# Optimization experiments

Measured on AMD Instinct MI355X. Metric: run time of the kernel, lower is better.

Reference implementation:

```python
import jax, jax.numpy as jnp
import numpy as np

K = 3  # kernel_size / number of adjacency partitions


def setup_inputs() -> dict:
    key = jax.random.key(0)
    k1, k2, k3 = jax.random.split(key, 3)
    N, C_in, T, V = 64, 64, 300, 25
    C_out = 64
    x = jax.random.normal(k1, (N, C_in, T, V), dtype=jnp.float32)
    A = jax.random.uniform(k2, (K, V, V), dtype=jnp.float32)
    W = jax.random.normal(k3, (C_in, K * C_out), dtype=jnp.float32) * 0.05
    b = jnp.zeros((K * C_out,), dtype=jnp.float32)
    return {"x": x, "A": A, "W": W, "b": b}


def reference(x, A, W, b):
    # 1x1 conv (channels_first) == per-position channel projection
    # x: [N, C_in, T, V], W: [C_in, K*C_out] -> y: [N, K*C_out, T, V]
    y = jnp.einsum('nitv,io->notv', x, W) + b[None, :, None, None]
    N, KC, T, V = y.shape
    C = KC // K
    y = y.reshape(N, K, C, T, V)
    # graph adjacency aggregation: [N,K,C,T,V] x [K,V,W] -> [N,C,T,W]
    out = jnp.einsum('nkctv,kvw->nctw', y, A)
    return (out, A)
```

## Files before the change

### kernel.cpp

```cpp
#include <hip/hip_runtime.h>
#include <hip/hip_bf16.h>


#define TT 3
#define TCHUNKS 100
#define NB 64
#define CI 64
#define TDIM 300
#define VDIM 25
#define CO 64
#define KK 3

#define XROWS (TT*32)
#define SMEM_BYTES (XROWS*128)

#define WBUF_BYTES (KK*4*2*64*16)
#define ABUF_BYTES (KK*2*64*16)

typedef __attribute__((ext_vector_type(8))) short bf16x8;
typedef __attribute__((ext_vector_type(4))) float f32x4;
typedef __attribute__((ext_vector_type(4))) int i32x4;
typedef __attribute__((ext_vector_type(4), aligned(4))) float f32x4u;

__device__ __forceinline__ unsigned int pack2(float lo, float hi) {
    __hip_bfloat162 h = __float22bfloat162_rn(make_float2(lo, hi));
    unsigned int u;
    __builtin_memcpy(&u, &h, 4);
    return u;
}
__device__ __forceinline__ unsigned short f2bf(float f) {
    __hip_bfloat16 h = __float2bfloat16(f);
    unsigned short u;
    __builtin_memcpy(&u, &h, 2);
    return u;
}

__global__ void sgcn_prep(const float* __restrict__ A, const float* __restrict__ W,
                          unsigned int* __restrict__ wbuf, unsigned int* __restrict__ abuf,
                          float* __restrict__ outA) {
    int id = blockIdx.x * 256 + threadIdx.x;
    if (id < KK * 4 * 2 * 64) {
        int l  = id & 63;
        int h  = (id >> 6) & 1;
        int wq = (id >> 7) & 3;
        int k  = id >> 9;
        int c  = wq * 16 + (l & 15);
        int ib = (l >> 4) * 8 + h * 32;
        unsigned int pk[4];
        #pragma unroll
        for (int j = 0; j < 4; ++j)
            pk[j] = pack2(W[(size_t)(ib + 2*j)     * (KK*CO) + k*CO + c],
                          W[(size_t)(ib + 2*j + 1) * (KK*CO) + k*CO + c]);
        *(uint4*)(wbuf + id * 4) = make_uint4(pk[0], pk[1], pk[2], pk[3]);
    }
    if (id < KK * 2 * 64) {
        int l  = id & 63;
        int nt = (id >> 6) & 1;
        int k  = id >> 7;
        int w  = nt * 16 + (l & 15);
        int vb = (l >> 4) * 8;
        unsigned int pk[4];
        #pragma unroll
        for (int j = 0; j < 4; ++j) {
            int v0 = vb + 2*j, v1 = v0 + 1;
            unsigned short u0 = (v0 < VDIM && w < VDIM) ? f2bf(A[k*VDIM*VDIM + v0*VDIM + w]) : (unsigned short)0;
            unsigned short u1 = (v1 < VDIM && w < VDIM) ? f2bf(A[k*VDIM*VDIM + v1*VDIM + w]) : (unsigned short)0;
            pk[j] = (unsigned int)u0 | ((unsigned int)u1 << 16);
        }
        *(uint4*)(abuf + id * 4) = make_uint4(pk[0], pk[1], pk[2], pk[3]);
    }
    if (id < KK * VDIM * VDIM) outA[id] = A[id];
}

__global__ __launch_bounds__(256, 4) void sgcn_fused(
    const float* __restrict__ x, const float* __restrict__ b,
    const unsigned int* __restrict__ wbuf, const unsigned int* __restrict__ abuf,
    float* __restrict__ out)
{
    __shared__ __align__(16) char smem[SMEM_BYTES];
    const int tid  = threadIdx.x;
    const int lane = tid & 63;
    const int wid  = tid >> 6;
    const int n    = blockIdx.y;
    const int t0   = blockIdx.x * TT;
    const int l15  = lane & 15;
    const int g    = lane >> 4;
    const int i0   = g * 8;
    const int c    = wid * 16 + l15;

    f32x4 q0[3], q1[3];
    #pragma unroll
    for (int j = 0; j < 3; ++j) {
        int id  = tid + j * 256;
        int i2  = id / 24;
        int rem = id - i2 * 24;
        int t   = rem >> 3;
        int grp = rem & 7;
        const float* pc0 = x + (((size_t)n * CI + 2*i2) * TDIM + (t0 + t)) * VDIM + 4*grp;
        const float* pc1 = pc0 + TDIM * VDIM;
        q0[j] = (f32x4){0.f, 0.f, 0.f, 0.f};
        q1[j] = (f32x4){0.f, 0.f, 0.f, 0.f};
        if (grp < 6) {
            q0[j] = *(const f32x4u*)pc0;
            q1[j] = *(const f32x4u*)pc1;
        } else if (grp == 6) {
            q0[j].x = pc0[0];
            q1[j].x = pc1[0];
        }
    }

    bf16x8 WB[KK][2], AB[KK][2];
    float bv[KK];
    #pragma unroll
    for (int k = 0; k < KK; ++k) {
        WB[k][0] = *(const bf16x8*)(wbuf + (((k*4 + wid)*2 + 0)*64 + lane)*4);
        WB[k][1] = *(const bf16x8*)(wbuf + (((k*4 + wid)*2 + 1)*64 + lane)*4);
        AB[k][0] = *(const bf16x8*)(abuf + ((k*2 + 0)*64 + lane)*4);
        AB[k][1] = *(const bf16x8*)(abuf + ((k*2 + 1)*64 + lane)*4);
        bv[k]    = b[k*CO + c];
    }

    #pragma unroll
    for (int j = 0; j < 3; ++j) {
        int id  = tid + j * 256;
        int i2  = id / 24;
        int rem = id - i2 * 24;
        int t   = rem >> 3;
        int grp = rem & 7;
        int rr0 = ((grp & 1) << 4) + ((grp >> 1) << 2);
        int rbase = t * 32 + rr0;
        int m   = rr0 & 7;
        #pragma unroll
        for (int p = 0; p < 4; ++p) {
            int fx = ((m + p) & 7) ^ t;
            int addr = (rbase + p) * 128 + ((4*i2) ^ (fx << 4));
            *(unsigned int*)(smem + addr) = pack2(q0[j][p], q1[j][p]);
        }
    }
    __syncthreads();

    const size_t cs = (size_t)TDIM * VDIM;
    #pragma unroll
    for (int t = 0; t < TT; ++t) {
        int j0 = t*32 + l15;
        int j1 = j0 + 16;
        const char* p0 = smem + j0*128;
        const char* p1 = smem + j1*128;
        int fx = ((l15 & 7) ^ t) << 4;
        bf16x8 A00 = *(const bf16x8*)(p0 + ((2*i0)      ^ fx));
        bf16x8 A01 = *(const bf16x8*)(p0 + ((2*i0 + 64) ^ fx));
        bf16x8 A10 = *(const bf16x8*)(p1 + ((2*i0)      ^ fx));
        bf16x8 A11 = *(const bf16x8*)(p1 + ((2*i0 + 64) ^ fx));

        f32x4 accA = {0.f, 0.f, 0.f, 0.f};
        f32x4 accB = {0.f, 0.f, 0.f, 0.f};
        #pragma unroll
        for (int k = 0; k < KK; ++k) {
            f32x4 D0 = {bv[k], bv[k], bv[k], bv[k]};
            f32x4 D1 = D0;
            D0 = __builtin_amdgcn_mfma_f32_16x16x32_bf16(A00, WB[k][0], D0, 0, 0, 0);
            D0 = __builtin_amdgcn_mfma_f32_16x16x32_bf16(A01, WB[k][1], D0, 0, 0, 0);
            D1 = __builtin_amdgcn_mfma_f32_16x16x32_bf16(A10, WB[k][0], D1, 0, 0, 0);
            D1 = __builtin_amdgcn_mfma_f32_16x16x32_bf16(A11, WB[k][1], D1, 0, 0, 0);
            i32x4 pav = {(int)pack2(D0.x, D0.y), (int)pack2(D0.z, D0.w),
                         (int)pack2(D1.x, D1.y), (int)pack2(D1.z, D1.w)};
            bf16x8 PA = __builtin_bit_cast(bf16x8, pav);
            accA = __builtin_amdgcn_mfma_f32_16x16x32_bf16(PA, AB[k][0], accA, 0, 0, 0);
            accB = __builtin_amdgcn_mfma_f32_16x16x32_bf16(PA, AB[k][1], accB, 0, 0, 0);
        }
        size_t base = (((size_t)n * CO + (wid*16 + 4*g)) * TDIM + (t0 + t)) * VDIM + l15;
        out[base]        = accA.x;
        out[base + cs]   = accA.y;
        out[base + 2*cs] = accA.z;
        out[base + 3*cs] = accA.w;
        if (l15 < VDIM - 16) {
            size_t base2 = base + 16;
            out[base2]        = accB.x;
            out[base2 + cs]   = accB.y;
            out[base2 + 2*cs] = accB.z;
            out[base2 + 3*cs] = accB.w;
        }
    }
}

extern "C" void kernel_launch(void* const* d_in, const int* in_sizes, int n_in,
                              void* d_out, int out_size, void* d_ws, size_t ws_size,
                              hipStream_t stream) {
    const float* x = (const float*)d_in[0];
    const float* A = (const float*)d_in[1];
    const float* W = (const float*)d_in[2];
    const float* b = (const float*)d_in[3];
    float* out = (float*)d_out;

    unsigned int* wbuf = (unsigned int*)d_ws;
    unsigned int* abuf = (unsigned int*)((char*)d_ws + WBUF_BYTES);

    const size_t out_elems = (size_t)NB * CO * TDIM * VDIM;
    sgcn_prep<<<8, 256, 0, stream>>>(A, W, wbuf, abuf, out + out_elems);

    dim3 grid(TCHUNKS, NB);
    sgcn_fused<<<grid, 256, 0, stream>>>(x, b, wbuf, abuf, out);
}
```

Baseline: 64.85 us.

## Double-buffer x tiles in shared memory to overlap next-chunk loads with compute

Each block now covers two chunks of six timesteps and uses two shared-memory buffers. Global loads for the second chunk are issued before the first chunk's MFMA work, then written to the second buffer afterwards. The aim is to hide global load latency behind compute and to cut the number of blocks. In exchange it needs more registers, 48KB of LDS per block and a lower launch-bounds occupancy of 2 blocks, with only 1600 blocks in the grid.

```diff
diff --git a/kernel.cpp b/kernel.cpp
--- a/kernel.cpp
+++ b/kernel.cpp
@@ -2,8 +2,9 @@
 #include <hip/hip_bf16.h>
 
 
-#define TT 3
-#define TCHUNKS 100
+#define TT 6
+#define NCHUNK 2
+#define GRIDX 25
 #define NB 64
 #define CI 64
 #define TDIM 300
@@ -72,42 +73,62 @@
     if (id < KK * VDIM * VDIM) outA[id] = A[id];
 }
 
-__global__ __launch_bounds__(256, 4) void sgcn_fused(
+__global__ __launch_bounds__(256, 2) void sgcn_fused(
     const float* __restrict__ x, const float* __restrict__ b,
     const unsigned int* __restrict__ wbuf, const unsigned int* __restrict__ abuf,
     float* __restrict__ out)
 {
-    __shared__ __align__(16) char smem[SMEM_BYTES];
+    __shared__ __align__(16) char smem[2][SMEM_BYTES];
     const int tid  = threadIdx.x;
     const int lane = tid & 63;
     const int wid  = tid >> 6;
     const int n    = blockIdx.y;
-    const int t0   = blockIdx.x * TT;
+    const int t0   = blockIdx.x * (TT * NCHUNK);
     const int l15  = lane & 15;
     const int g    = lane >> 4;
     const int i0   = g * 8;
     const int c    = wid * 16 + l15;
 
-    f32x4 q0[3], q1[3];
-    #pragma unroll
-    for (int j = 0; j < 3; ++j) {
-        int id  = tid + j * 256;
-        int i2  = id / 24;
-        int rem = id - i2 * 24;
-        int t   = rem >> 3;
-        int grp = rem & 7;
-        const float* pc0 = x + (((size_t)n * CI + 2*i2) * TDIM + (t0 + t)) * VDIM + 4*grp;
-        const float* pc1 = pc0 + TDIM * VDIM;
-        q0[j] = (f32x4){0.f, 0.f, 0.f, 0.f};
-        q1[j] = (f32x4){0.f, 0.f, 0.f, 0.f};
-        if (grp < 6) {
-            q0[j] = *(const f32x4u*)pc0;
-            q1[j] = *(const f32x4u*)pc1;
-        } else if (grp == 6) {
-            q0[j].x = pc0[0];
-            q1[j].x = pc1[0];
-        }
-    }
+    float q0[6][4], q1[6][4];
+
+    #define STAGE_LOAD(TBASE)                                                        \
+        _Pragma("unroll")                                                            \
+        for (int j = 0; j < 6; ++j) {                                                \
+            int id  = tid + j * 256;                                                 \
+            int i2  = id / 48;                                                       \
+            int rem = id - i2 * 48;                                                  \
+            int t   = rem >> 3;                                                      \
+            int grp = rem & 7;                                                       \
+            const float* pc0 = x + (((size_t)n * CI + 2*i2) * TDIM + ((TBASE) + t)) * VDIM + 4*grp; \
+            const float* pc1 = pc0 + TDIM * VDIM;                                    \
+            f32x4 a0 = {0.f, 0.f, 0.f, 0.f};                                         \
+            f32x4 a1 = {0.f, 0.f, 0.f, 0.f};                                         \
+            if (grp < 6)      { a0 = *(const f32x4u*)pc0; a1 = *(const f32x4u*)pc1; }\
+            else if (grp == 6){ a0.x = pc0[0];            a1.x = pc1[0]; }           \
+            q0[j][0]=a0.x; q0[j][1]=a0.y; q0[j][2]=a0.z; q0[j][3]=a0.w;              \
+            q1[j][0]=a1.x; q1[j][1]=a1.y; q1[j][2]=a1.z; q1[j][3]=a1.w;              \
+        }
+
+    #define STAGE_WRITE(BUF)                                                         \
+        _Pragma("unroll")                                                            \
+        for (int j = 0; j < 6; ++j) {                                                \
+            int id  = tid + j * 256;                                                 \
+            int i2  = id / 48;                                                       \
+            int rem = id - i2 * 48;                                                  \
+            int t   = rem >> 3;                                                      \
+            int grp = rem & 7;                                                       \
+            int rr0 = ((grp & 1) << 4) + ((grp >> 1) << 2);                          \
+            int rbase = t * 32 + rr0;                                                \
+            int m   = rr0 & 7;                                                       \
+            _Pragma("unroll")                                                        \
+            for (int p = 0; p < 4; ++p) {                                            \
+                int fx = ((m + p) & 7) ^ t;                                          \
+                int addr = (rbase + p) * 128 + ((4*i2) ^ (fx << 4));                 \
+                *(unsigned int*)((BUF) + addr) = pack2(q0[j][p], q1[j][p]);          \
+            }                                                                        \
+        }
+
+    STAGE_LOAD(t0);
 
     bf16x8 WB[KK][2], AB[KK][2];
     float bv[KK];
@@ -120,67 +141,67 @@
         bv[k]    = b[k*CO + c];
     }
 
+    STAGE_WRITE(&smem[0][0]);
+    __syncthreads();
+
+    const size_t cs = (size_t)TDIM * VDIM;
+
     #pragma unroll
-    for (int j = 0; j < 3; ++j) {
-        int id  = tid + j * 256;
-        int i2  = id / 24;
-        int rem = id - i2 * 24;
-        int t   = rem >> 3;
-        int grp = rem & 7;
-        int rr0 = ((grp & 1) << 4) + ((grp >> 1) << 2);
-        int rbase = t * 32 + rr0;
-        int m   = rr0 & 7;
+    for (int ch = 0; ch < NCHUNK; ++ch) {
+        const char* rbuf = &smem[ch][0];
+        const int   tg0  = t0 + ch * TT;
+
+        if (ch == 0) STAGE_LOAD(t0 + TT);
+
         #pragma unroll
-        for (int p = 0; p < 4; ++p) {
-            int fx = ((m + p) & 7) ^ t;
-            int addr = (rbase + p) * 128 + ((4*i2) ^ (fx << 4));
-            *(unsigned int*)(smem + addr) = pack2(q0[j][p], q1[j][p]);
-        }
-    }
-    __syncthreads();
-
-    const size_t cs = (size_t)TDIM * VDIM;
-    #pragma unroll
-    for (int t = 0; t < TT; ++t) {
-        int j0 = t*32 + l15;
-        int j1 = j0 + 16;
-        const char* p0 = smem + j0*128;
-        const char* p1 = smem + j1*128;
-        int fx = ((l15 & 7) ^ t) << 4;
-        bf16x8 A00 = *(const bf16x8*)(p0 + ((2*i0)      ^ fx));
-        bf16x8 A01 = *(const bf16x8*)(p0 + ((2*i0 + 64) ^ fx));
-        bf16x8 A10 = *(const bf16x8*)(p1 + ((2*i0)      ^ fx));
-        bf16x8 A11 = *(const bf16x8*)(p1 + ((2*i0 + 64) ^ fx));
-
-        f32x4 accA = {0.f, 0.f, 0.f, 0.f};
-        f32x4 accB = {0.f, 0.f, 0.f, 0.f};
-        #pragma unroll
-        for (int k = 0; k < KK; ++k) {
-            f32x4 D0 = {bv[k], bv[k], bv[k], bv[k]};
-            f32x4 D1 = D0;
-            D0 = __builtin_amdgcn_mfma_f32_16x16x32_bf16(A00, WB[k][0], D0, 0, 0, 0);
-            D0 = __builtin_amdgcn_mfma_f32_16x16x32_bf16(A01, WB[k][1], D0, 0, 0, 0);
-            D1 = __builtin_amdgcn_mfma_f32_16x16x32_bf16(A10, WB[k][0], D1, 0, 0, 0);
-            D1 = __builtin_amdgcn_mfma_f32_16x16x32_bf16(A11, WB[k][1], D1, 0, 0, 0);
-            i32x4 pav = {(int)pack2(D0.x, D0.y), (int)pack2(D0.z, D0.w),
-                         (int)pack2(D1.x, D1.y), (int)pack2(D1.z, D1.w)};
-            bf16x8 PA = __builtin_bit_cast(bf16x8, pav);
-            accA = __builtin_amdgcn_mfma_f32_16x16x32_bf16(PA, AB[k][0], accA, 0, 0, 0);
-            accB = __builtin_amdgcn_mfma_f32_16x16x32_bf16(PA, AB[k][1], accB, 0, 0, 0);
-        }
-        size_t base = (((size_t)n * CO + (wid*16 + 4*g)) * TDIM + (t0 + t)) * VDIM + l15;
-        out[base]        = accA.x;
-        out[base + cs]   = accA.y;
-        out[base + 2*cs] = accA.z;
-        out[base + 3*cs] = accA.w;
-        if (l15 < VDIM - 16) {
-            size_t base2 = base + 16;
-            out[base2]        = accB.x;
-            out[base2 + cs]   = accB.y;
-            out[base2 + 2*cs] = accB.z;
-            out[base2 + 3*cs] = accB.w;
-        }
-    }
+        for (int t = 0; t < TT; ++t) {
+            int j0 = t*32 + l15;
+            int j1 = j0 + 16;
+            const char* p0 = rbuf + j0*128;
+            const char* p1 = rbuf + j1*128;
+            int fx = ((l15 & 7) ^ t) << 4;
+            bf16x8 A00 = *(const bf16x8*)(p0 + ((2*i0)      ^ fx));
+            bf16x8 A01 = *(const bf16x8*)(p0 + ((2*i0 + 64) ^ fx));
+            bf16x8 A10 = *(const bf16x8*)(p1 + ((2*i0)      ^ fx));
+            bf16x8 A11 = *(const bf16x8*)(p1 + ((2*i0 + 64) ^ fx));
+
+            f32x4 accA = {0.f, 0.f, 0.f, 0.f};
+            f32x4 accB = {0.f, 0.f, 0.f, 0.f};
+            #pragma unroll
+            for (int k = 0; k < KK; ++k) {
+                f32x4 D0 = {bv[k], bv[k], bv[k], bv[k]};
+                f32x4 D1 = D0;
+                D0 = __builtin_amdgcn_mfma_f32_16x16x32_bf16(A00, WB[k][0], D0, 0, 0, 0);
+                D0 = __builtin_amdgcn_mfma_f32_16x16x32_bf16(A01, WB[k][1], D0, 0, 0, 0);
+                D1 = __builtin_amdgcn_mfma_f32_16x16x32_bf16(A10, WB[k][0], D1, 0, 0, 0);
+                D1 = __builtin_amdgcn_mfma_f32_16x16x32_bf16(A11, WB[k][1], D1, 0, 0, 0);
+                i32x4 pav = {(int)pack2(D0.x, D0.y), (int)pack2(D0.z, D0.w),
+                             (int)pack2(D1.x, D1.y), (int)pack2(D1.z, D1.w)};
+                bf16x8 PA = __builtin_bit_cast(bf16x8, pav);
+                accA = __builtin_amdgcn_mfma_f32_16x16x32_bf16(PA, AB[k][0], accA, 0, 0, 0);
+                accB = __builtin_amdgcn_mfma_f32_16x16x32_bf16(PA, AB[k][1], accB, 0, 0, 0);
+            }
+            size_t base = (((size_t)n * CO + (wid*16 + 4*g)) * TDIM + (tg0 + t)) * VDIM + l15;
+            out[base]        = accA.x;
+            out[base + cs]   = accA.y;
+            out[base + 2*cs] = accA.z;
+            out[base + 3*cs] = accA.w;
+            if (l15 < VDIM - 16) {
+                size_t base2 = base + 16;
+                out[base2]        = accB.x;
+                out[base2 + cs]   = accB.y;
+                out[base2 + 2*cs] = accB.z;
+                out[base2 + 3*cs] = accB.w;
+            }
+        }
+
+        if (ch == 0) {
+            STAGE_WRITE(&smem[1][0]);
+            __syncthreads();
+        }
+    }
+    #undef STAGE_LOAD
+    #undef STAGE_WRITE
 }
 
 extern "C" void kernel_launch(void* const* d_in, const int* in_sizes, int n_in,
@@ -198,6 +219,6 @@
     const size_t out_elems = (size_t)NB * CO * TDIM * VDIM;
     sgcn_prep<<<8, 256, 0, stream>>>(A, W, wbuf, abuf, out + out_elems);
 
-    dim3 grid(TCHUNKS, NB);
+    dim3 grid(GRIDX, NB);
     sgcn_fused<<<grid, 256, 0, stream>>>(x, b, wbuf, abuf, out);
 }
```

Result: faster. 59.27 us (-8.6%).
